# Performance work log

Measured on AMD Instinct MI355X. Metric: run time of the kernel, lower is better.

Reference implementation:

```python
import jax, jax.numpy as jnp
import numpy as np

E = 1024
H = 16
D = E // H  # head_dim = 64


def setup_inputs() -> dict:
    key = jax.random.key(0)
    k_x, k_w1, k_b1, k_w2, k_b2 = jax.random.split(key, 5)
    s = 1.0 / np.sqrt(E)
    return {
        "x": jax.random.normal(k_x, (2, 2048, E), dtype=jnp.float32),
        "qkv_w": jax.random.uniform(k_w1, (3 * E, E), jnp.float32, -s, s),
        "qkv_b": jax.random.uniform(k_b1, (3 * E,), jnp.float32, -s, s),
        "out_w": jax.random.uniform(k_w2, (E, E), jnp.float32, -s, s),
        "out_b": jax.random.uniform(k_b2, (E,), jnp.float32, -s, s),
    }


def reference(x, qkv_w, qkv_b, out_w, out_b):
    B, T, _ = x.shape
    # qkv projection (torch Linear: x @ W.T + b)
    qkv = x @ qkv_w.T + qkv_b  # [B, T, 3E]
    q, k, v = jnp.split(qkv, 3, axis=-1)
    # [B, T, E] -> [B, H, T, D]
    def to_heads(t):
        return t.reshape(B, T, H, D).transpose(0, 2, 1, 3)
    q, k, v = to_heads(q), to_heads(k), to_heads(v)
    scale = 1.0 / np.sqrt(D).astype(np.float32)
    scores = jnp.einsum("bhqd,bhkd->bhqk", q, k) * scale  # [B, H, T, T]
    attn = jax.nn.softmax(scores, axis=-1)
    # dropout is identity in eval mode
    out = jnp.einsum("bhqk,bhkd->bhqd", attn, v)  # [B, H, T, D]
    out = out.transpose(0, 2, 1, 3).reshape(B, T, E)
    return out @ out_w.T + out_b
```

## Files before the change

### kernel.cpp

```cpp
#include <hip/hip_runtime.h>

#define TT 2048
#define BB 2
#define EE 1024
#define HH 16
#define DD 64
#define E3 3072
#define NTOK 4096

typedef unsigned short u16;
typedef _Float16 __attribute__((ext_vector_type(8))) half8;
typedef _Float16 __attribute__((ext_vector_type(4))) half4;
typedef __fp16 __attribute__((ext_vector_type(2))) fp16x2;
typedef __attribute__((ext_vector_type(4))) float f32x4;

__device__ __forceinline__ unsigned f2h(float f) {
    union { _Float16 h; u16 u; } v; v.h = (_Float16)f; return (unsigned)v.u;
}
__device__ __forceinline__ fp16x2 pk2(float a, float b) {
    return __builtin_amdgcn_cvt_pkrtz(a, b);
}

__device__ __forceinline__ void async_ld16(const u16* g, const u16* l) {
    auto gp = reinterpret_cast<const __attribute__((address_space(1))) unsigned*>(
        reinterpret_cast<uintptr_t>(g));
    auto lp = reinterpret_cast<__attribute__((address_space(3))) unsigned*>(
        reinterpret_cast<uintptr_t>(l));
    __builtin_amdgcn_global_load_lds(gp, lp, 16, 0, 0);
}

__global__ __launch_bounds__(256) void split3(
    const float* __restrict__ x, const float* __restrict__ w1,
    const float* __restrict__ w2,
    u16* __restrict__ xh, u16* __restrict__ w1h, u16* __restrict__ w2h)
{
    const int N1 = (NTOK * EE) / 4;
    const int N2 = N1 + (E3 * EE) / 4;
    int i = blockIdx.x * 256 + threadIdx.x;
    const float* src; u16* dst; int j;
    if (i < N1)      { src = x;  dst = xh;  j = i; }
    else if (i < N2) { src = w1; dst = w1h; j = i - N1; }
    else             { src = w2; dst = w2h; j = i - N2; }
    float4 v = ((const float4*)src)[j];
    *(uint2*)&dst[(size_t)j * 4] = make_uint2(
        f2h(v.x) | (f2h(v.y) << 16), f2h(v.z) | (f2h(v.w) << 16));
}

__global__ __launch_bounds__(256) void vtrans(
    const u16* __restrict__ qkv, u16* __restrict__ vt)
{
    __shared__ u16 L[64][72];
    const int tid = threadIdx.x;
    const int t0 = blockIdx.x * 64;
    const int h  = blockIdx.y;
    const int b  = blockIdx.z;
    const int row = tid >> 2;
    const int c16 = (tid & 3) << 4;

    const u16* src = qkv + (size_t)(b * TT + t0 + row) * E3 + 2 * EE + h * DD + c16;
    *(uint4*)&L[row][c16]     = *(const uint4*)src;
    *(uint4*)&L[row][c16 + 8] = *(const uint4*)(src + 8);
    __syncthreads();

    union { uint4 u[2]; u16 s[16]; } P;
#pragma unroll
    for (int j = 0; j < 16; ++j) P.s[j] = L[c16 + j][row];
    u16* dst = vt + ((size_t)(b * HH + h) * DD + row) * TT + t0 + c16;
    *(uint4*)dst       = P.u[0];
    *(uint4*)(dst + 8) = P.u[1];
}

template <int WMT, bool QSCALE, bool F16OUT>
__global__ __launch_bounds__(256, 3) void gemm_f16(
    const u16* __restrict__ Ag, const u16* __restrict__ Wg,
    const float* __restrict__ bias, void* __restrict__ Cout, int M, int N)
{
    constexpr int BM = WMT * 32;
    constexpr int APASS = BM / 32;
    __shared__ u16 sA[BM * 64];
    __shared__ u16 sB[128 * 64];

    const int tid  = threadIdx.x;
    const int lane = tid & 63;
    const int wave = tid >> 6;
    const int quad = lane >> 4;
    const int l16  = lane & 15;
    const int wm = wave >> 1, wn = wave & 1;
    const int m0 = blockIdx.y * BM;
    const int n0 = blockIdx.x * 128;

    const int srow = tid >> 3;
    const int schk = tid & 7;

    const u16* ag[APASS]; int aldw[APASS];
#pragma unroll
    for (int p = 0; p < APASS; ++p) {
        int row = p * 32 + srow;
        ag[p] = Ag + (size_t)(m0 + row) * EE + ((schk ^ (row & 7)) << 3);
        aldw[p] = (p * 256 + wave * 64) * 8;
    }
    const u16* bg[4]; int bldw[4];
#pragma unroll
    for (int p = 0; p < 4; ++p) {
        int row = p * 32 + srow;
        bg[p] = Wg + (size_t)(n0 + row) * EE + ((schk ^ (row & 7)) << 3);
        bldw[p] = (p * 256 + wave * 64) * 8;
    }

    f32x4 acc[WMT][4];
#pragma unroll
    for (int mt = 0; mt < WMT; ++mt)
#pragma unroll
        for (int nt = 0; nt < 4; ++nt) acc[mt][nt] = (f32x4){0.f, 0.f, 0.f, 0.f};

    for (int k0 = 0; k0 < EE; k0 += 64) {
        __syncthreads();
#pragma unroll
        for (int p = 0; p < APASS; ++p) async_ld16(ag[p] + k0, sA + aldw[p]);
#pragma unroll
        for (int p = 0; p < 4; ++p)    async_ld16(bg[p] + k0, sB + bldw[p]);
        __syncthreads();

        half8 fa[WMT][2], fb[4][2];
#pragma unroll
        for (int mt = 0; mt < WMT; ++mt) {
            int r = wm * (WMT * 16) + mt * 16 + l16;
#pragma unroll
            for (int ks = 0; ks < 2; ++ks)
                fa[mt][ks] = *(const half8*)&sA[r * 64 + (((ks * 4 + quad) ^ (r & 7)) << 3)];
        }
#pragma unroll
        for (int nt = 0; nt < 4; ++nt) {
            int r = wn * 64 + nt * 16 + l16;
#pragma unroll
            for (int ks = 0; ks < 2; ++ks)
                fb[nt][ks] = *(const half8*)&sB[r * 64 + (((ks * 4 + quad) ^ (r & 7)) << 3)];
        }
#pragma unroll
        for (int ks = 0; ks < 2; ++ks)
#pragma unroll
            for (int mt = 0; mt < WMT; ++mt)
#pragma unroll
                for (int nt = 0; nt < 4; ++nt)
                    acc[mt][nt] = __builtin_amdgcn_mfma_f32_16x16x32_f16(
                        fa[mt][ks], fb[nt][ks], acc[mt][nt], 0, 0, 0);
    }

    const float scale = (QSCALE && n0 < EE) ? 0.18033688011112042f : 1.0f;
    float bv[4];
#pragma unroll
    for (int nt = 0; nt < 4; ++nt) bv[nt] = bias[n0 + wn * 64 + nt * 16 + l16];
#pragma unroll
    for (int mt = 0; mt < WMT; ++mt)
#pragma unroll
        for (int nt = 0; nt < 4; ++nt)
#pragma unroll
            for (int r = 0; r < 4; ++r) {
                int rg = m0 + wm * (WMT * 16) + mt * 16 + quad * 4 + r;
                int cg = n0 + wn * 64 + nt * 16 + l16;
                float v = (acc[mt][nt][r] + bv[nt]) * scale;
                if (F16OUT) ((u16*)Cout)[(size_t)rg * N + cg] = (u16)f2h(v);
                else        ((float*)Cout)[(size_t)rg * N + cg] = v;
            }
}

__global__ __launch_bounds__(128, 2) void attn_mfma(
    const u16* __restrict__ qkv, const u16* __restrict__ vt,
    u16* __restrict__ obuf)
{
    __shared__ u16 KB[2][64][64];
    __shared__ u16 VB[2][64][64];

    const int tid  = threadIdx.x;
    const int wave = tid >> 6;
    const int lane = tid & 63;
    const int quad = lane >> 4;
    const int l16  = lane & 15;

    const int q0 = blockIdx.x * 64;
    const int hh = blockIdx.y;
    const int b  = blockIdx.z;

    const int srow = tid >> 3;
    const int schk = tid & 7;
    const int ldsw = wave * 512;

    half8 qb[2][2];
#pragma unroll
    for (int qt = 0; qt < 2; ++qt) {
        int row = q0 + wave * 32 + qt * 16 + l16;
        const u16* qg = qkv + (size_t)(b * TT + row) * E3 + hh * DD;
#pragma unroll
        for (int ks = 0; ks < 2; ++ks)
            qb[qt][ks] = *(const half8*)(qg + ks * 32 + quad * 8);
    }

#pragma unroll
    for (int p = 0; p < 4; ++p) {
        int row = p * 16 + srow;
        int sw8 = (schk ^ (row & 7)) << 3;
        async_ld16(qkv + (size_t)(b * TT + row) * E3 + EE + hh * DD + sw8,
                   &KB[0][0][0] + p * 1024 + ldsw);
        async_ld16(vt + ((size_t)(b * HH + hh) * DD + row) * TT + sw8,
                   &VB[0][0][0] + p * 1024 + ldsw);
    }
    __syncthreads();

    const f32x4 Z = {0.f, 0.f, 0.f, 0.f};
    float l_i[2] = {0.f, 0.f};
    f32x4 o[4][2];
#pragma unroll
    for (int dt = 0; dt < 4; ++dt)
#pragma unroll
        for (int qt = 0; qt < 2; ++qt) o[dt][qt] = (f32x4){0.f, 0.f, 0.f, 0.f};

    int cur = 0;
    for (int kt = 0; kt < TT; kt += 64, cur ^= 1) {
        const int ktn = (kt + 64) & (TT - 1);
#pragma unroll
        for (int p = 0; p < 4; ++p) {
            int row = p * 16 + srow;
            int sw8 = (schk ^ (row & 7)) << 3;
            async_ld16(qkv + (size_t)(b * TT + ktn + row) * E3 + EE + hh * DD + sw8,
                       &KB[cur ^ 1][0][0] + p * 1024 + ldsw);
            async_ld16(vt + ((size_t)(b * HH + hh) * DD + row) * TT + ktn + sw8,
                       &VB[cur ^ 1][0][0] + p * 1024 + ldsw);
        }

#pragma unroll
        for (int kg = 0; kg < 4; ++kg) {
            int r0 = kg * 16 + l16;
            half8 kf0 = *(const half8*)&KB[cur][r0][((quad)     ^ (r0 & 7)) << 3];
            half8 kf1 = *(const half8*)&KB[cur][r0][((4 + quad) ^ (r0 & 7)) << 3];

            half4 pb[2];
#pragma unroll
            for (int qt = 0; qt < 2; ++qt) {
                f32x4 t = __builtin_amdgcn_mfma_f32_16x16x32_f16(kf0, qb[qt][0], Z, 0, 0, 0);
                f32x4 s = __builtin_amdgcn_mfma_f32_16x16x32_f16(kf1, qb[qt][1], t, 0, 0, 0);
                float p0 = __builtin_amdgcn_exp2f(s[0]);
                float p1 = __builtin_amdgcn_exp2f(s[1]);
                float p2 = __builtin_amdgcn_exp2f(s[2]);
                float p3 = __builtin_amdgcn_exp2f(s[3]);
                l_i[qt] += (p0 + p1) + (p2 + p3);
                union { fp16x2 h[2]; half4 v; } u;
                u.h[0] = pk2(p0, p1);
                u.h[1] = pk2(p2, p3);
                pb[qt] = u.v;
            }
#pragma unroll
            for (int dt = 0; dt < 4; ++dt) {
                int vr = dt * 16 + l16;
                int chunk = (kg * 2 + (quad >> 1)) ^ (vr & 7);
                half4 vf = *(const half4*)&VB[cur][vr][chunk * 8 + ((quad & 1) << 2)];
                o[dt][0] = __builtin_amdgcn_mfma_f32_16x16x16f16(vf, pb[0], o[dt][0], 0, 0, 0);
                o[dt][1] = __builtin_amdgcn_mfma_f32_16x16x16f16(vf, pb[1], o[dt][1], 0, 0, 0);
            }
        }

        __syncthreads();
    }

    float inv[2];
#pragma unroll
    for (int qt = 0; qt < 2; ++qt) {
        float l = l_i[qt];
        l += __shfl_xor(l, 16, 64);
        l += __shfl_xor(l, 32, 64);
        inv[qt] = 1.f / l;
    }
#pragma unroll
    for (int qt = 0; qt < 2; ++qt) {
        size_t base = (size_t)(b * TT + q0 + wave * 32 + qt * 16 + l16) * EE + hh * DD;
#pragma unroll
        for (int dt = 0; dt < 4; ++dt) {
            unsigned hv[4];
#pragma unroll
            for (int r = 0; r < 4; ++r) hv[r] = f2h(o[dt][qt][r] * inv[qt]);
            *(uint2*)&obuf[base + dt * 16 + quad * 4] =
                make_uint2(hv[0] | (hv[1] << 16), hv[2] | (hv[3] << 16));
        }
    }
}

extern "C" void kernel_launch(void* const* d_in, const int* in_sizes, int n_in,
                              void* d_out, int out_size, void* d_ws, size_t ws_size,
                              hipStream_t stream)
{
    const float* x     = (const float*)d_in[0];
    const float* qkv_w = (const float*)d_in[1];
    const float* qkv_b = (const float*)d_in[2];
    const float* out_w = (const float*)d_in[3];
    const float* out_b = (const float*)d_in[4];
    float* out = (float*)d_out;

    const size_t NX  = (size_t)NTOK * EE;
    const size_t NW1 = (size_t)E3 * EE;
    const size_t NW2 = (size_t)EE * EE;
    const size_t NQ  = (size_t)NTOK * E3;

    u16* ws   = (u16*)d_ws;
    u16* x_h  = ws;
    u16* w1h  = ws + NX;
    u16* w2h  = w1h + NW1;
    u16* qkvb = w2h + NW2;
    u16* vtb  = qkvb + NQ;

    split3<<<dim3((unsigned)((NX + NW1 + NW2) / 4 / 256)), 256, 0, stream>>>(
        x, qkv_w, out_w, x_h, w1h, w2h);

    gemm_f16<4, true, true><<<dim3(E3 / 128, NTOK / 128), 256, 0, stream>>>(
        x_h, w1h, qkv_b, (void*)qkvb, NTOK, E3);

    vtrans<<<dim3(TT / 64, HH, BB), 256, 0, stream>>>(qkvb, vtb);

    attn_mfma<<<dim3(TT / 64, HH, BB), 128, 0, stream>>>(qkvb, vtb, x_h);

    gemm_f16<2, false, false><<<dim3(EE / 128, NTOK / 64), 256, 0, stream>>>(
        x_h, w2h, out_b, (void*)out, NTOK, EE);
}
```

Before: 188.2 us.

## Enlarge attention tiles to 128 queries and 128 keys per iteration

The attention kernel now uses 256-thread blocks covering 128 queries, and each loop iteration processes 128 keys instead of 64. This halves the number of K/V tile loads per query and the number of barriers. QK^T scores for all 8 key groups are computed before the PV MFMAs, and the V tile gets a 16-chunk XOR swizzle. In exchange, LDS use doubles to 64KB per block and the buffered probabilities raise register pressure, which may lower occupancy. The grid also has half as many blocks.

```diff
diff --git a/kernel.cpp b/kernel.cpp
--- a/kernel.cpp
+++ b/kernel.cpp
@@ -164,12 +164,12 @@
             }
 }
 
-__global__ __launch_bounds__(128, 2) void attn_mfma(
+__global__ __launch_bounds__(256, 2) void attn_mfma(
     const u16* __restrict__ qkv, const u16* __restrict__ vt,
     u16* __restrict__ obuf)
 {
-    __shared__ u16 KB[2][64][64];
-    __shared__ u16 VB[2][64][64];
+    __shared__ u16 KB[2][128][64];
+    __shared__ u16 VB[2][64][128];
 
     const int tid  = threadIdx.x;
     const int wave = tid >> 6;
@@ -177,13 +177,15 @@
     const int quad = lane >> 4;
     const int l16  = lane & 15;
 
-    const int q0 = blockIdx.x * 64;
+    const int q0 = blockIdx.x * 128;
     const int hh = blockIdx.y;
     const int b  = blockIdx.z;
 
-    const int srow = tid >> 3;
-    const int schk = tid & 7;
-    const int ldsw = wave * 512;
+    const int srow  = tid >> 3;
+    const int schk  = tid & 7;
+    const int vsrow = tid >> 4;
+    const int vschk = tid & 15;
+    const int ldsw  = wave * 512;
 
     half8 qb[2][2];
 #pragma unroll
@@ -197,12 +199,14 @@
 
 #pragma unroll
     for (int p = 0; p < 4; ++p) {
-        int row = p * 16 + srow;
-        int sw8 = (schk ^ (row & 7)) << 3;
-        async_ld16(qkv + (size_t)(b * TT + row) * E3 + EE + hh * DD + sw8,
-                   &KB[0][0][0] + p * 1024 + ldsw);
-        async_ld16(vt + ((size_t)(b * HH + hh) * DD + row) * TT + sw8,
-                   &VB[0][0][0] + p * 1024 + ldsw);
+        int krow = p * 32 + srow;
+        async_ld16(qkv + (size_t)(b * TT + krow) * E3 + EE + hh * DD
+                       + ((schk ^ (krow & 7)) << 3),
+                   &KB[0][0][0] + p * 2048 + ldsw);
+        int vrow = p * 16 + vsrow;
+        async_ld16(vt + ((size_t)(b * HH + hh) * DD + vrow) * TT
+                      + ((vschk ^ (vrow & 15)) << 3),
+                   &VB[0][0][0] + p * 2048 + ldsw);
     }
     __syncthreads();
 
@@ -215,25 +219,26 @@
         for (int qt = 0; qt < 2; ++qt) o[dt][qt] = (f32x4){0.f, 0.f, 0.f, 0.f};
 
     int cur = 0;
-    for (int kt = 0; kt < TT; kt += 64, cur ^= 1) {
-        const int ktn = (kt + 64) & (TT - 1);
+    for (int kt = 0; kt < TT; kt += 128, cur ^= 1) {
+        const int ktn = (kt + 128) & (TT - 1);
 #pragma unroll
         for (int p = 0; p < 4; ++p) {
-            int row = p * 16 + srow;
-            int sw8 = (schk ^ (row & 7)) << 3;
-            async_ld16(qkv + (size_t)(b * TT + ktn + row) * E3 + EE + hh * DD + sw8,
-                       &KB[cur ^ 1][0][0] + p * 1024 + ldsw);
-            async_ld16(vt + ((size_t)(b * HH + hh) * DD + row) * TT + ktn + sw8,
-                       &VB[cur ^ 1][0][0] + p * 1024 + ldsw);
-        }
-
-#pragma unroll
-        for (int kg = 0; kg < 4; ++kg) {
+            int krow = p * 32 + srow;
+            async_ld16(qkv + (size_t)(b * TT + ktn + krow) * E3 + EE + hh * DD
+                           + ((schk ^ (krow & 7)) << 3),
+                       &KB[cur ^ 1][0][0] + p * 2048 + ldsw);
+            int vrow = p * 16 + vsrow;
+            async_ld16(vt + ((size_t)(b * HH + hh) * DD + vrow) * TT + ktn
+                          + ((vschk ^ (vrow & 15)) << 3),
+                       &VB[cur ^ 1][0][0] + p * 2048 + ldsw);
+        }
+
+        half4 pb[2][8];
+#pragma unroll
+        for (int kg = 0; kg < 8; ++kg) {
             int r0 = kg * 16 + l16;
             half8 kf0 = *(const half8*)&KB[cur][r0][((quad)     ^ (r0 & 7)) << 3];
             half8 kf1 = *(const half8*)&KB[cur][r0][((4 + quad) ^ (r0 & 7)) << 3];
-
-            half4 pb[2];
 #pragma unroll
             for (int qt = 0; qt < 2; ++qt) {
                 f32x4 t = __builtin_amdgcn_mfma_f32_16x16x32_f16(kf0, qb[qt][0], Z, 0, 0, 0);
@@ -246,15 +251,20 @@
                 union { fp16x2 h[2]; half4 v; } u;
                 u.h[0] = pk2(p0, p1);
                 u.h[1] = pk2(p2, p3);
-                pb[qt] = u.v;
+                pb[qt][kg] = u.v;
             }
+        }
+
+#pragma unroll
+        for (int kg = 0; kg < 8; ++kg) {
+            int c = kg * 2 + (quad >> 1);
 #pragma unroll
             for (int dt = 0; dt < 4; ++dt) {
                 int vr = dt * 16 + l16;
-                int chunk = (kg * 2 + (quad >> 1)) ^ (vr & 7);
-                half4 vf = *(const half4*)&VB[cur][vr][chunk * 8 + ((quad & 1) << 2)];
-                o[dt][0] = __builtin_amdgcn_mfma_f32_16x16x16f16(vf, pb[0], o[dt][0], 0, 0, 0);
-                o[dt][1] = __builtin_amdgcn_mfma_f32_16x16x16f16(vf, pb[1], o[dt][1], 0, 0, 0);
+                half4 vf = *(const half4*)&VB[cur][vr]
+                               [((c ^ l16) << 3) + ((quad & 1) << 2)];
+                o[dt][0] = __builtin_amdgcn_mfma_f32_16x16x16f16(vf, pb[0][kg], o[dt][0], 0, 0, 0);
+                o[dt][1] = __builtin_amdgcn_mfma_f32_16x16x16f16(vf, pb[1][kg], o[dt][1], 0, 0, 0);
             }
         }
 
@@ -314,7 +324,7 @@
 
     vtrans<<<dim3(TT / 64, HH, BB), 256, 0, stream>>>(qkvb, vtb);
 
-    attn_mfma<<<dim3(TT / 64, HH, BB), 128, 0, stream>>>(qkvb, vtb, x_h);
+    attn_mfma<<<dim3(TT / 128, HH, BB), 256, 0, stream>>>(qkvb, vtb, x_h);
 
     gemm_f16<2, false, false><<<dim3(EE / 128, NTOK / 64), 256, 0, stream>>>(
         x_h, w2h, out_b, (void*)out, NTOK, EE);
```

Result: no change. 189.5 us (+0.7%).
